# Kernel tuning notes

Hardware: AMD Instinct MI355X
Metric: run time of the kernel (lower is better)

Reference implementation:

```python
import jax, jax.numpy as jnp
import numpy as np

B, S, H = 64, 1024, 512
NEG = -1e10


def setup_inputs() -> dict:
    key = jax.random.key(0)
    ks = jax.random.split(key, 10)
    hidden = jax.random.normal(ks[0], (B, H), dtype=jnp.float32)
    encoder_outputs = jax.random.normal(ks[1], (S, B, H), dtype=jnp.float32)
    attn_mask = jax.random.randint(ks[2], (B, S), 0, 2, dtype=jnp.int32)
    src_gps_seqs = jax.random.uniform(ks[3], (S, B, 2), dtype=jnp.float32)
    src = jax.random.uniform(ks[4], (S, B, 3), dtype=jnp.float32)
    src_rids = jax.random.randint(ks[5], (S, B, 1), 0, 10000, dtype=jnp.int64)
    input_id = jax.random.randint(ks[6], (B, 1), 0, 10000, dtype=jnp.int64)
    trg_gps_seqs = jax.random.uniform(ks[7], (B, 2), dtype=jnp.float32)
    # learned params: attn = Linear(2H -> H), v = Linear(H -> 1, no bias)
    bound = 1.0 / np.sqrt(2 * H)
    attn_w = jax.random.uniform(ks[8], (H, 2 * H), minval=-bound, maxval=bound, dtype=jnp.float32)
    attn_b = jnp.zeros((H,), dtype=jnp.float32)
    v_w = jax.random.uniform(ks[9], (1, H), minval=-1.0 / np.sqrt(H), maxval=1.0 / np.sqrt(H), dtype=jnp.float32)
    return {"t": 0, "hidden": hidden, "encoder_outputs": encoder_outputs,
            "attn_mask": attn_mask, "src_gps_seqs": src_gps_seqs, "src": src,
            "src_rids": src_rids, "input_id": input_id, "trg_gps_seqs": trg_gps_seqs,
            "attn_w": attn_w, "attn_b": attn_b, "v_w": v_w}


def reference(t, hidden, encoder_outputs, attn_mask, src_gps_seqs, src,
              src_rids, input_id, trg_gps_seqs, attn_w, attn_b, v_w):
    # encoder_outputs: [S, B, H] -> [B, S, H]
    enc = jnp.transpose(encoder_outputs, (1, 0, 2))
    s_len = enc.shape[1]
    # hidden [B, H] broadcast over src_len -> [B, S, H]
    h = jnp.broadcast_to(hidden[:, None, :], (hidden.shape[0], s_len, hidden.shape[1]))
    cat = jnp.concatenate([h, enc], axis=2)                      # [B, S, 2H]
    energy = jnp.tanh(jnp.einsum('bsk,hk->bsh', cat, attn_w) + attn_b)  # [B, S, H]
    attention = jnp.einsum('bsh,oh->bs', energy, v_w)            # [B, S]
    attention = jnp.where(attn_mask == 0, jnp.float32(NEG), attention)
    return jax.nn.softmax(attention, axis=1)
```

## Files before the change

### kernel.cpp

```cpp
#include <hip/hip_runtime.h>
#include <hip/hip_bf16.h>

typedef unsigned short ushort_t;
typedef unsigned int uint_t;
typedef __attribute__((ext_vector_type(8))) short short8;
typedef __attribute__((ext_vector_type(4))) float f32x4;

#define NEG_VAL -1e10f

#define GL16(gp, lp) __builtin_amdgcn_global_load_lds( \
    (const __attribute__((address_space(1))) uint_t*)(gp), \
    (__attribute__((address_space(3))) uint_t*)(lp), 16, 0, 0)

__device__ __forceinline__ ushort_t f2bf(float x) {
    uint_t u = __float_as_uint(x);
    uint_t r = (u + 0x7fffu + ((u >> 16) & 1u)) >> 16;
    return (ushort_t)r;
}

__device__ __forceinline__ uint_t pkbf(float a, float b) {
    return (uint_t)f2bf(a) | ((uint_t)f2bf(b) << 16);
}

__device__ __forceinline__ float tanh_fast(float x) {
    float e = __expf(2.0f * x);
    return 1.0f - 2.0f / (e + 1.0f);
}

__global__ void w2conv_kernel(const float* __restrict__ attn_w, ushort_t* __restrict__ w2) {
    int gid = blockIdx.x * 256 + threadIdx.x;
    int h = gid >> 7, q = gid & 127;
    float4 v = *(const float4*)(attn_w + (size_t)h * 1024 + 512 + q * 4);
    uint2 p;
    p.x = pkbf(v.x, v.y);
    p.y = pkbf(v.z, v.w);
    *(uint2*)(w2 + h * 512 + q * 4) = p;
}

__global__ void hproj_kernel(const float* __restrict__ hidden,
                             const float* __restrict__ attn_w,
                             const float* __restrict__ attn_b,
                             float* __restrict__ hb) {
    int gid = blockIdx.x * 256 + threadIdx.x;
    int b = gid >> 9, h = gid & 511;
    const float4* hp = (const float4*)(hidden + (size_t)b * 512);
    const float4* wp = (const float4*)(attn_w + (size_t)h * 1024);
    float a0 = 0.f, a1 = 0.f, a2 = 0.f, a3 = 0.f;
    #pragma unroll 4
    for (int i = 0; i < 128; i += 4) {
        float4 x0 = hp[i + 0], w0 = wp[i + 0];
        a0 += x0.x * w0.x + x0.y * w0.y + x0.z * w0.z + x0.w * w0.w;
        float4 x1 = hp[i + 1], w1 = wp[i + 1];
        a1 += x1.x * w1.x + x1.y * w1.y + x1.z * w1.z + x1.w * w1.w;
        float4 x2 = hp[i + 2], w2v = wp[i + 2];
        a2 += x2.x * w2v.x + x2.y * w2v.y + x2.z * w2v.z + x2.w * w2v.w;
        float4 x3 = hp[i + 3], w3 = wp[i + 3];
        a3 += x3.x * w3.x + x3.y * w3.y + x3.z * w3.z + x3.w * w3.w;
    }
    hb[gid] = attn_b[h] + ((a0 + a1) + (a2 + a3));
}

__global__ __launch_bounds__(512, 2) void gemm_kernel(
    const float* __restrict__ enc,
    const ushort_t* __restrict__ w2,
    const float* __restrict__ hb,
    const float* __restrict__ vw,
    float* __restrict__ logits)
{
    __shared__ __align__(16) float As[3][128 * 32];
    __shared__ __align__(16) ushort_t Bs[3][512 * 32];
    __shared__ float red[4][128];

    const int tid = threadIdx.x;
    const int wv = tid >> 6, l = tid & 63;
    const int wm = wv >> 2, wn = wv & 3;
    const int lr = l & 15, lq = l >> 4;
    const size_t m0 = (size_t)blockIdx.x * 128;

    const float* aG[2];
    uint_t aL[2];
    #pragma unroll
    for (int i = 0; i < 2; i++) {
        int u = 512 * i + 64 * wv + l;
        int row = u >> 3;
        int j = (l & 7) ^ (l >> 3);
        aG[i] = enc + (m0 + row) * 512 + j * 4;
        aL[i] = (uint_t)(512 * i + 64 * wv) * 16;
    }
    const ushort_t* bG[4];
    uint_t bL[4];
    #pragma unroll
    for (int i = 0; i < 4; i++) {
        int u = 512 * i + 64 * wv + l;
        int row = u >> 2;
        int j = (l & 3) ^ ((l >> 3) & 3);
        bG[i] = w2 + (size_t)row * 512 + j * 8;
        bL[i] = (uint_t)(512 * i + 64 * wv) * 16;
    }

    uint_t aoffL[4], aoffH[4], boff[8];
    #pragma unroll
    for (int mf = 0; mf < 4; mf++) {
        int row = wm * 64 + mf * 16 + lr;
        aoffL[mf] = (uint_t)row * 128 + (uint_t)(((lq * 2 + 0) ^ (row & 7)) * 16);
        aoffH[mf] = (uint_t)row * 128 + (uint_t)(((lq * 2 + 1) ^ (row & 7)) * 16);
    }
    #pragma unroll
    for (int nf = 0; nf < 8; nf++) {
        int r = wn * 128 + nf * 16 + lr;
        boff[nf] = (uint_t)r * 64 + (uint_t)((lq ^ ((r >> 1) & 3)) * 16);
    }

    #define STAGE(kt, buf) do { \
        _Pragma("unroll") \
        for (int i = 0; i < 2; i++) GL16(aG[i] + (kt) * 32, (char*)(&As[(buf)][0]) + aL[i]); \
        _Pragma("unroll") \
        for (int i = 0; i < 4; i++) GL16(bG[i] + (kt) * 32, (char*)(&Bs[(buf)][0]) + bL[i]); \
    } while (0)

    STAGE(0, 0);
    STAGE(1, 1);
    asm volatile("s_waitcnt vmcnt(6)" ::: "memory");
    __builtin_amdgcn_sched_barrier(0);
    __builtin_amdgcn_s_barrier();

    f32x4 acc[4][8] = {};

    #pragma unroll
    for (int kt = 0; kt < 16; ++kt) {
        const int cur = kt % 3;
        short8 af[4], bfr[8];
        #pragma unroll
        for (int nf = 0; nf < 8; nf++)
            bfr[nf] = *(const short8*)((const char*)(&Bs[cur][0]) + boff[nf]);
        #pragma unroll
        for (int mf = 0; mf < 4; mf++) {
            f32x4 lo = *(const f32x4*)((const char*)(&As[cur][0]) + aoffL[mf]);
            f32x4 hi = *(const f32x4*)((const char*)(&As[cur][0]) + aoffH[mf]);
            union { short8 s; uint_t u[4]; } t;
            t.u[0] = pkbf(lo[0], lo[1]);
            t.u[1] = pkbf(lo[2], lo[3]);
            t.u[2] = pkbf(hi[0], hi[1]);
            t.u[3] = pkbf(hi[2], hi[3]);
            af[mf] = t.s;
        }
        asm volatile("s_waitcnt lgkmcnt(0)" ::: "memory");
        __builtin_amdgcn_sched_barrier(0);
        __builtin_amdgcn_s_barrier();
        if (kt + 2 <= 15) {
            const int nb = (kt + 2) % 3;
            STAGE(kt + 2, nb);
        }
        #pragma unroll
        for (int mf = 0; mf < 4; mf++)
            #pragma unroll
            for (int nf = 0; nf < 8; nf++)
                acc[mf][nf] = __builtin_amdgcn_mfma_f32_16x16x32_bf16(af[mf], bfr[nf], acc[mf][nf], 0, 0, 0);
        if (kt < 15) {
            if (kt < 14) { asm volatile("s_waitcnt vmcnt(6)" ::: "memory"); }
            else         { asm volatile("s_waitcnt vmcnt(0)" ::: "memory"); }
            __builtin_amdgcn_sched_barrier(0);
            __builtin_amdgcn_s_barrier();
        }
    }
    #undef STAGE

    float vv[8];
    #pragma unroll
    for (int nf = 0; nf < 8; nf++) vv[nf] = vw[wn * 128 + nf * 16 + lr];

    #pragma unroll
    for (int mf = 0; mf < 4; mf++) {
        #pragma unroll
        for (int r = 0; r < 4; r++) {
            int row = wm * 64 + mf * 16 + lq * 4 + r;
            int b = row & 63;
            const float* hbp = hb + b * 512 + wn * 128 + lr;
            float p = 0.f;
            #pragma unroll
            for (int nf = 0; nf < 8; nf++) {
                float x = acc[mf][nf][r] + hbp[nf * 16];
                p += tanh_fast(x) * vv[nf];
            }
            p += __shfl_xor(p, 1);
            p += __shfl_xor(p, 2);
            p += __shfl_xor(p, 4);
            p += __shfl_xor(p, 8);
            if (lr == 0) red[wn][row] = p;
        }
    }
    __syncthreads();
    if (tid < 128) {
        logits[m0 + tid] = (red[0][tid] + red[1][tid]) + (red[2][tid] + red[3][tid]);
    }
}

__global__ void softmax_kernel(const float* __restrict__ logits,
                               const int* __restrict__ mask,
                               float* __restrict__ out) {
    __shared__ float sred[8];
    int b = blockIdx.x;
    int t = threadIdx.x;
    float vals[4];
    float mx = -INFINITY;
    #pragma unroll
    for (int i = 0; i < 4; i++) {
        int s = t + i * 256;
        float x = logits[s * 64 + b];
        if (mask[b * 1024 + s] == 0) x = NEG_VAL;
        vals[i] = x;
        mx = fmaxf(mx, x);
    }
    #pragma unroll
    for (int o = 32; o; o >>= 1) mx = fmaxf(mx, __shfl_xor(mx, o));
    int w = t >> 6;
    if ((t & 63) == 0) sred[w] = mx;
    __syncthreads();
    mx = fmaxf(fmaxf(sred[0], sred[1]), fmaxf(sred[2], sred[3]));
    float sum = 0.f;
    #pragma unroll
    for (int i = 0; i < 4; i++) {
        vals[i] = __expf(vals[i] - mx);
        sum += vals[i];
    }
    #pragma unroll
    for (int o = 32; o; o >>= 1) sum += __shfl_xor(sum, o);
    if ((t & 63) == 0) sred[4 + w] = sum;
    __syncthreads();
    float tot = (sred[4] + sred[5]) + (sred[6] + sred[7]);
    float inv = 1.0f / tot;
    #pragma unroll
    for (int i = 0; i < 4; i++) out[b * 1024 + t + i * 256] = vals[i] * inv;
}

extern "C" void kernel_launch(void* const* d_in, const int* in_sizes, int n_in,
                              void* d_out, int out_size, void* d_ws, size_t ws_size,
                              hipStream_t stream) {
    const float* hidden = (const float*)d_in[1];
    const float* enc    = (const float*)d_in[2];
    const int*   mask   = (const int*)d_in[3];
    const float* attn_w = (const float*)d_in[9];
    const float* attn_b = (const float*)d_in[10];
    const float* vw     = (const float*)d_in[11];
    float* out = (float*)d_out;

    char* ws = (char*)d_ws;
    ushort_t* w2  = (ushort_t*)ws;
    float* hb     = (float*)(ws + 512 * 1024);
    float* logits = (float*)(ws + 640 * 1024);

    w2conv_kernel<<<256, 256, 0, stream>>>(attn_w, w2);
    hproj_kernel<<<128, 256, 0, stream>>>(hidden, attn_w, attn_b, hb);
    gemm_kernel<<<512, 512, 0, stream>>>(enc, w2, hb, vw, logits);
    softmax_kernel<<<64, 256, 0, stream>>>(logits, mask, out);
}
```

Measured before the change: 108.8 us.

## Split GEMM N dimension across two blocks with XCD-aware mapping and double buffering

The fused GEMM+tanh+v-projection kernel now uses 256-thread blocks, each covering 128 rows by 256 of the 512 hidden columns. That doubles the grid to 1024 blocks and writes two partial logit arrays, which the softmax kernel sums. Block IDs are remapped so that the two N-halves of the same M tile, and neighbouring M tiles, land on the same XCD for L2 reuse of the encoder tile. The triple-buffered pipeline with hand-placed waitcnts is replaced by simple double buffering and __syncthreads, trading some memory latency hiding for more blocks and smaller LDS per block. The encoder A tile is now read twice from global memory, once per N-half.

Result: faster. 100.0 us (-8.1%).

```diff
diff --git a/kernel.cpp b/kernel.cpp
--- a/kernel.cpp
+++ b/kernel.cpp
@@ -60,42 +60,45 @@
     hb[gid] = attn_b[h] + ((a0 + a1) + (a2 + a3));
 }
 
-__global__ __launch_bounds__(512, 2) void gemm_kernel(
+__global__ __launch_bounds__(256, 2) void gemm_kernel(
     const float* __restrict__ enc,
     const ushort_t* __restrict__ w2,
     const float* __restrict__ hb,
     const float* __restrict__ vw,
-    float* __restrict__ logits)
+    float* __restrict__ part)
 {
-    __shared__ __align__(16) float As[3][128 * 32];
-    __shared__ __align__(16) ushort_t Bs[3][512 * 32];
-    __shared__ float red[4][128];
+    __shared__ __align__(16) float As[2][128 * 32];
+    __shared__ __align__(16) ushort_t Bs[2][256 * 32];
+    __shared__ float red[2][128];
 
     const int tid = threadIdx.x;
+    const int bid = blockIdx.x;
+    const int xcd = bid & 7, j = bid >> 3;
+    const int mt = xcd * 64 + (j >> 1), nt = j & 1;
+    const size_t m0 = (size_t)mt * 128;
+    const int h0 = nt * 256;
+
     const int wv = tid >> 6, l = tid & 63;
-    const int wm = wv >> 2, wn = wv & 3;
+    const int wm = wv >> 1, wn = wv & 1;
     const int lr = l & 15, lq = l >> 4;
-    const size_t m0 = (size_t)blockIdx.x * 128;
-
-    const float* aG[2];
-    uint_t aL[2];
-    #pragma unroll
-    for (int i = 0; i < 2; i++) {
-        int u = 512 * i + 64 * wv + l;
-        int row = u >> 3;
-        int j = (l & 7) ^ (l >> 3);
-        aG[i] = enc + (m0 + row) * 512 + j * 4;
-        aL[i] = (uint_t)(512 * i + 64 * wv) * 16;
+
+    const float* aG[4];
+    uint_t aL[4];
+    #pragma unroll
+    for (int i = 0; i < 4; i++) {
+        int rowA = i * 32 + wv * 8 + (l >> 3);
+        int jA = (l & 7) ^ (l >> 3);
+        aG[i] = enc + (m0 + rowA) * 512 + jA * 4;
+        aL[i] = (uint_t)(i * 256 + wv * 64) * 16;
     }
     const ushort_t* bG[4];
     uint_t bL[4];
     #pragma unroll
     for (int i = 0; i < 4; i++) {
-        int u = 512 * i + 64 * wv + l;
-        int row = u >> 2;
-        int j = (l & 3) ^ ((l >> 3) & 3);
-        bG[i] = w2 + (size_t)row * 512 + j * 8;
-        bL[i] = (uint_t)(512 * i + 64 * wv) * 16;
+        int rowB = i * 64 + wv * 16 + (l >> 2);
+        int jB = (l & 3) ^ ((l >> 3) & 3);
+        bG[i] = w2 + (size_t)(h0 + rowB) * 512 + jB * 8;
+        bL[i] = (uint_t)(i * 256 + wv * 64) * 16;
     }
 
     uint_t aoffL[4], aoffH[4], boff[8];
@@ -113,22 +116,20 @@
 
     #define STAGE(kt, buf) do { \
         _Pragma("unroll") \
-        for (int i = 0; i < 2; i++) GL16(aG[i] + (kt) * 32, (char*)(&As[(buf)][0]) + aL[i]); \
+        for (int i = 0; i < 4; i++) GL16(aG[i] + (kt) * 32, (char*)(&As[(buf)][0]) + aL[i]); \
         _Pragma("unroll") \
         for (int i = 0; i < 4; i++) GL16(bG[i] + (kt) * 32, (char*)(&Bs[(buf)][0]) + bL[i]); \
     } while (0)
 
     STAGE(0, 0);
-    STAGE(1, 1);
-    asm volatile("s_waitcnt vmcnt(6)" ::: "memory");
-    __builtin_amdgcn_sched_barrier(0);
-    __builtin_amdgcn_s_barrier();
+    __syncthreads();
 
     f32x4 acc[4][8] = {};
 
-    #pragma unroll
+    #pragma unroll 2
     for (int kt = 0; kt < 16; ++kt) {
-        const int cur = kt % 3;
+        const int cur = kt & 1;
+        if (kt < 15) STAGE(kt + 1, cur ^ 1);
         short8 af[4], bfr[8];
         #pragma unroll
         for (int nf = 0; nf < 8; nf++)
@@ -144,30 +145,18 @@
             t.u[3] = pkbf(hi[2], hi[3]);
             af[mf] = t.s;
         }
-        asm volatile("s_waitcnt lgkmcnt(0)" ::: "memory");
-        __builtin_amdgcn_sched_barrier(0);
-        __builtin_amdgcn_s_barrier();
-        if (kt + 2 <= 15) {
-            const int nb = (kt + 2) % 3;
-            STAGE(kt + 2, nb);
-        }
         #pragma unroll
         for (int mf = 0; mf < 4; mf++)
             #pragma unroll
             for (int nf = 0; nf < 8; nf++)
                 acc[mf][nf] = __builtin_amdgcn_mfma_f32_16x16x32_bf16(af[mf], bfr[nf], acc[mf][nf], 0, 0, 0);
-        if (kt < 15) {
-            if (kt < 14) { asm volatile("s_waitcnt vmcnt(6)" ::: "memory"); }
-            else         { asm volatile("s_waitcnt vmcnt(0)" ::: "memory"); }
-            __builtin_amdgcn_sched_barrier(0);
-            __builtin_amdgcn_s_barrier();
-        }
+        __syncthreads();
     }
     #undef STAGE
 
     float vv[8];
     #pragma unroll
-    for (int nf = 0; nf < 8; nf++) vv[nf] = vw[wn * 128 + nf * 16 + lr];
+    for (int nf = 0; nf < 8; nf++) vv[nf] = vw[h0 + wn * 128 + nf * 16 + lr];
 
     #pragma unroll
     for (int mf = 0; mf < 4; mf++) {
@@ -175,7 +164,7 @@
         for (int r = 0; r < 4; r++) {
             int row = wm * 64 + mf * 16 + lq * 4 + r;
             int b = row & 63;
-            const float* hbp = hb + b * 512 + wn * 128 + lr;
+            const float* hbp = hb + b * 512 + h0 + wn * 128 + lr;
             float p = 0.f;
             #pragma unroll
             for (int nf = 0; nf < 8; nf++) {
@@ -191,11 +180,11 @@
     }
     __syncthreads();
     if (tid < 128) {
-        logits[m0 + tid] = (red[0][tid] + red[1][tid]) + (red[2][tid] + red[3][tid]);
-    }
-}
-
-__global__ void softmax_kernel(const float* __restrict__ logits,
+        part[(size_t)nt * 65536 + m0 + tid] = red[0][tid] + red[1][tid];
+    }
+}
+
+__global__ void softmax_kernel(const float* __restrict__ part,
                                const int* __restrict__ mask,
                                float* __restrict__ out) {
     __shared__ float sred[8];
@@ -206,7 +195,8 @@
     #pragma unroll
     for (int i = 0; i < 4; i++) {
         int s = t + i * 256;
-        float x = logits[s * 64 + b];
+        int row = s * 64 + b;
+        float x = part[row] + part[65536 + row];
         if (mask[b * 1024 + s] == 0) x = NEG_VAL;
         vals[i] = x;
         mx = fmaxf(mx, x);
@@ -245,12 +235,12 @@
     float* out = (float*)d_out;
 
     char* ws = (char*)d_ws;
-    ushort_t* w2  = (ushort_t*)ws;
-    float* hb     = (float*)(ws + 512 * 1024);
-    float* logits = (float*)(ws + 640 * 1024);
+    ushort_t* w2 = (ushort_t*)ws;
+    float* hb   = (float*)(ws + 512 * 1024);
+    float* part = (float*)(ws + 640 * 1024);
 
     w2conv_kernel<<<256, 256, 0, stream>>>(attn_w, w2);
     hproj_kernel<<<128, 256, 0, stream>>>(hidden, attn_w, attn_b, hb);
-    gemm_kernel<<<512, 512, 0, stream>>>(enc, w2, hb, vw, logits);
-    softmax_kernel<<<64, 256, 0, stream>>>(logits, mask, out);
-}
+    gemm_kernel<<<1024, 256, 0, stream>>>(enc, w2, hb, vw, part);
+    softmax_kernel<<<64, 256, 0, stream>>>(part, mask, out);
+}
```

## Load GEMM operands directly from global memory into registers, bypassing LDS

Applied to the files above, without the earlier changes.

Drops the LDS triple-buffered staging with global_load_lds and barriers. Each wave now loads its A (fp32 encoder rows) and B (bf16 weights) fragments straight from global memory into registers, software-prefetching the next A tile. It also switches the bf16 conversion to the hardware v_cvt_pk_bf16_f32 instruction and relaxes launch bounds to one block per CU, allowing more registers. The aim is to remove barrier and LDS traffic. The cost is redundant global and L2 reads, because waves sharing rows or columns each fetch them separately. The per-lane loads are also less coalesced, and occupancy is lower.

After: 178.9 us. 1.64x slower.

```diff
diff --git a/kernel.cpp b/kernel.cpp
--- a/kernel.cpp
+++ b/kernel.cpp
@@ -8,10 +8,6 @@
 
 #define NEG_VAL -1e10f
 
-#define GL16(gp, lp) __builtin_amdgcn_global_load_lds( \
-    (const __attribute__((address_space(1))) uint_t*)(gp), \
-    (__attribute__((address_space(3))) uint_t*)(lp), 16, 0, 0)
-
 __device__ __forceinline__ ushort_t f2bf(float x) {
     uint_t u = __float_as_uint(x);
     uint_t r = (u + 0x7fffu + ((u >> 16) & 1u)) >> 16;
@@ -20,6 +16,12 @@
 
 __device__ __forceinline__ uint_t pkbf(float a, float b) {
     return (uint_t)f2bf(a) | ((uint_t)f2bf(b) << 16);
+}
+
+__device__ __forceinline__ uint_t cvtpk(float a, float b) {
+    uint_t r;
+    asm("v_cvt_pk_bf16_f32 %0, %1, %2" : "=v"(r) : "v"(a), "v"(b));
+    return r;
 }
 
 __device__ __forceinline__ float tanh_fast(float x) {
@@ -60,15 +62,13 @@
     hb[gid] = attn_b[h] + ((a0 + a1) + (a2 + a3));
 }
 
-__global__ __launch_bounds__(512, 2) void gemm_kernel(
+__global__ __launch_bounds__(512, 1) void gemm_kernel(
     const float* __restrict__ enc,
     const ushort_t* __restrict__ w2,
     const float* __restrict__ hb,
     const float* __restrict__ vw,
     float* __restrict__ logits)
 {
-    __shared__ __align__(16) float As[3][128 * 32];
-    __shared__ __align__(16) ushort_t Bs[3][512 * 32];
     __shared__ float red[4][128];
 
     const int tid = threadIdx.x;
@@ -77,93 +77,57 @@
     const int lr = l & 15, lq = l >> 4;
     const size_t m0 = (size_t)blockIdx.x * 128;
 
-    const float* aG[2];
-    uint_t aL[2];
-    #pragma unroll
-    for (int i = 0; i < 2; i++) {
-        int u = 512 * i + 64 * wv + l;
-        int row = u >> 3;
-        int j = (l & 7) ^ (l >> 3);
-        aG[i] = enc + (m0 + row) * 512 + j * 4;
-        aL[i] = (uint_t)(512 * i + 64 * wv) * 16;
-    }
-    const ushort_t* bG[4];
-    uint_t bL[4];
-    #pragma unroll
-    for (int i = 0; i < 4; i++) {
-        int u = 512 * i + 64 * wv + l;
-        int row = u >> 2;
-        int j = (l & 3) ^ ((l >> 3) & 3);
-        bG[i] = w2 + (size_t)row * 512 + j * 8;
-        bL[i] = (uint_t)(512 * i + 64 * wv) * 16;
-    }
-
-    uint_t aoffL[4], aoffH[4], boff[8];
+    const float* aB[4];
+    #pragma unroll
+    for (int mf = 0; mf < 4; mf++)
+        aB[mf] = enc + (m0 + wm * 64 + mf * 16 + lr) * 512 + lq * 8;
+    const ushort_t* bB[8];
+    #pragma unroll
+    for (int nf = 0; nf < 8; nf++)
+        bB[nf] = w2 + (size_t)(wn * 128 + nf * 16 + lr) * 512 + lq * 8;
+
+    f32x4 acc[4][8] = {};
+
+    f32x4 a0[4], a1[4], n0[4], n1[4];
     #pragma unroll
     for (int mf = 0; mf < 4; mf++) {
-        int row = wm * 64 + mf * 16 + lr;
-        aoffL[mf] = (uint_t)row * 128 + (uint_t)(((lq * 2 + 0) ^ (row & 7)) * 16);
-        aoffH[mf] = (uint_t)row * 128 + (uint_t)(((lq * 2 + 1) ^ (row & 7)) * 16);
-    }
-    #pragma unroll
-    for (int nf = 0; nf < 8; nf++) {
-        int r = wn * 128 + nf * 16 + lr;
-        boff[nf] = (uint_t)r * 64 + (uint_t)((lq ^ ((r >> 1) & 3)) * 16);
-    }
-
-    #define STAGE(kt, buf) do { \
-        _Pragma("unroll") \
-        for (int i = 0; i < 2; i++) GL16(aG[i] + (kt) * 32, (char*)(&As[(buf)][0]) + aL[i]); \
-        _Pragma("unroll") \
-        for (int i = 0; i < 4; i++) GL16(bG[i] + (kt) * 32, (char*)(&Bs[(buf)][0]) + bL[i]); \
-    } while (0)
-
-    STAGE(0, 0);
-    STAGE(1, 1);
-    asm volatile("s_waitcnt vmcnt(6)" ::: "memory");
-    __builtin_amdgcn_sched_barrier(0);
-    __builtin_amdgcn_s_barrier();
-
-    f32x4 acc[4][8] = {};
+        a0[mf] = *(const f32x4*)(aB[mf]);
+        a1[mf] = *(const f32x4*)(aB[mf] + 4);
+    }
 
     #pragma unroll
     for (int kt = 0; kt < 16; ++kt) {
-        const int cur = kt % 3;
-        short8 af[4], bfr[8];
+        short8 bf[8];
         #pragma unroll
         for (int nf = 0; nf < 8; nf++)
-            bfr[nf] = *(const short8*)((const char*)(&Bs[cur][0]) + boff[nf]);
+            bf[nf] = *(const short8*)(bB[nf] + kt * 32);
+        if (kt < 15) {
+            #pragma unroll
+            for (int mf = 0; mf < 4; mf++) {
+                n0[mf] = *(const f32x4*)(aB[mf] + (kt + 1) * 32);
+                n1[mf] = *(const f32x4*)(aB[mf] + (kt + 1) * 32 + 4);
+            }
+        }
+        short8 af[4];
         #pragma unroll
         for (int mf = 0; mf < 4; mf++) {
-            f32x4 lo = *(const f32x4*)((const char*)(&As[cur][0]) + aoffL[mf]);
-            f32x4 hi = *(const f32x4*)((const char*)(&As[cur][0]) + aoffH[mf]);
             union { short8 s; uint_t u[4]; } t;
-            t.u[0] = pkbf(lo[0], lo[1]);
-            t.u[1] = pkbf(lo[2], lo[3]);
-            t.u[2] = pkbf(hi[0], hi[1]);
-            t.u[3] = pkbf(hi[2], hi[3]);
+            t.u[0] = cvtpk(a0[mf][0], a0[mf][1]);
+            t.u[1] = cvtpk(a0[mf][2], a0[mf][3]);
+            t.u[2] = cvtpk(a1[mf][0], a1[mf][1]);
+            t.u[3] = cvtpk(a1[mf][2], a1[mf][3]);
             af[mf] = t.s;
         }
-        asm volatile("s_waitcnt lgkmcnt(0)" ::: "memory");
-        __builtin_amdgcn_sched_barrier(0);
-        __builtin_amdgcn_s_barrier();
-        if (kt + 2 <= 15) {
-            const int nb = (kt + 2) % 3;
-            STAGE(kt + 2, nb);
-        }
         #pragma unroll
         for (int mf = 0; mf < 4; mf++)
             #pragma unroll
             for (int nf = 0; nf < 8; nf++)
-                acc[mf][nf] = __builtin_amdgcn_mfma_f32_16x16x32_bf16(af[mf], bfr[nf], acc[mf][nf], 0, 0, 0);
+                acc[mf][nf] = __builtin_amdgcn_mfma_f32_16x16x32_bf16(af[mf], bf[nf], acc[mf][nf], 0, 0, 0);
         if (kt < 15) {
-            if (kt < 14) { asm volatile("s_waitcnt vmcnt(6)" ::: "memory"); }
-            else         { asm volatile("s_waitcnt vmcnt(0)" ::: "memory"); }
-            __builtin_amdgcn_sched_barrier(0);
-            __builtin_amdgcn_s_barrier();
-        }
-    }
-    #undef STAGE
+            #pragma unroll
+            for (int mf = 0; mf < 4; mf++) { a0[mf] = n0[mf]; a1[mf] = n1[mf]; }
+        }
+    }
 
     float vv[8];
     #pragma unroll
```
